# Kernel optimization log

Hardware: AMD Instinct MI355X
Metric: run time of the kernel (lower is better)

Reference implementation:

```python
import jax, jax.numpy as jnp
import numpy as np

TOP_K = 2


def setup_inputs() -> dict:
    key = jax.random.key(0)
    ks = jax.random.split(key, 4)
    T, E, D_IN, D_H, D_OUT = 8192, 8, 1024, 4096, 1024
    s_in = 1.0 / np.sqrt(D_IN)
    s_h = 1.0 / np.sqrt(D_H)
    return {
        "x": jax.random.normal(ks[0], (T, D_IN), dtype=jnp.float32),
        "Wg": jax.random.normal(ks[1], (D_IN, E), dtype=jnp.float32) * s_in,
        "bg": jnp.zeros((E,), dtype=jnp.float32),
        "W1": jax.random.normal(ks[2], (E, D_IN, D_H), dtype=jnp.float32) * s_in,
        "b1": jnp.zeros((E, D_H), dtype=jnp.float32),
        "W2": jax.random.normal(ks[3], (E, D_H, D_OUT), dtype=jnp.float32) * s_h,
        "b2": jnp.zeros((E, D_OUT), dtype=jnp.float32),
    }


def moe_forward(x, Wg, bg, W1, b1, W2, b2):
    # Top-k gate: logits [T,E] -> top-k -> softmax over the k selected logits,
    # scattered back into a dense [T,E] weight matrix (zeros elsewhere).
    logits = x @ Wg + bg                              # [T, E]
    topv, topi = jax.lax.top_k(logits, TOP_K)         # [T, k]
    topw = jax.nn.softmax(topv, axis=-1)              # [T, k]
    T, E = logits.shape
    weights = jnp.zeros((T, E), dtype=logits.dtype)
    rows = jnp.arange(T)[:, None]
    weights = weights.at[rows, topi].set(topw)        # dense gate weights [T, E]

    # Dense all-expert MLP (faithful to the naive torch module):
    h = jax.nn.relu(jnp.einsum("ti,eih->teh", x, W1) + b1[None])   # [T, E, H]
    expert_out = jnp.einsum("teh,eho->teo", h, W2) + b2[None]      # [T, E, O]

    # Top-k weighted sum over experts.
    return jnp.einsum("te,teo->to", weights, expert_out)           # [T, O]


def reference(x, Wg, bg, W1, b1, W2, b2):
    return moe_forward(x, Wg, bg, W1, b1, W2, b2)
```

## Files before the change

### kernel.cpp

```cpp
#include <hip/hip_runtime.h>
#include <hip/hip_bf16.h>
#include <stdint.h>

#define NTOK 8192
#define NE 8
#define DIN 1024
#define DH 4096
#define DOUT 1024
#define MAXMB 135

typedef __bf16 bf16;
typedef __bf16 bf16_8 __attribute__((ext_vector_type(8)));
typedef __bf16 bf16_4 __attribute__((ext_vector_type(4)));
typedef float f32_4 __attribute__((ext_vector_type(4)));

__device__ __forceinline__ void gl_lds16(const void* g, void* l) {
  __builtin_amdgcn_global_load_lds(
      (const __attribute__((address_space(1))) unsigned int*)g,
      (__attribute__((address_space(3))) unsigned int*)l, 16, 0, 0);
}

__global__ void gate_kernel(const float* __restrict__ x, const float* __restrict__ Wg,
                            const float* __restrict__ bg,
                            int* __restrict__ topi, float* __restrict__ topw) {
  int t = blockIdx.x * 4 + (threadIdx.x >> 6);
  int lane = threadIdx.x & 63;
  float acc[NE];
#pragma unroll
  for (int e = 0; e < NE; e++) acc[e] = 0.f;
  const float* xr = x + (size_t)t * DIN;
#pragma unroll
  for (int i = 0; i < DIN / 64; i++) {
    float xv = xr[lane + 64 * i];
    const float4* wr = (const float4*)(Wg + (size_t)(lane + 64 * i) * NE);
    float4 w0 = wr[0], w1 = wr[1];
    acc[0] += xv * w0.x; acc[1] += xv * w0.y; acc[2] += xv * w0.z; acc[3] += xv * w0.w;
    acc[4] += xv * w1.x; acc[5] += xv * w1.y; acc[6] += xv * w1.z; acc[7] += xv * w1.w;
  }
#pragma unroll
  for (int off = 32; off > 0; off >>= 1)
#pragma unroll
    for (int e = 0; e < NE; e++) acc[e] += __shfl_xor(acc[e], off, 64);
  if (lane == 0) {
    float lg[NE];
#pragma unroll
    for (int e = 0; e < NE; e++) lg[e] = acc[e] + bg[e];
    int i0 = 0; float v0 = lg[0];
#pragma unroll
    for (int e = 1; e < NE; e++) if (lg[e] > v0) { v0 = lg[e]; i0 = e; }
    int i1 = -1; float v1 = -3.0e38f;
#pragma unroll
    for (int e = 0; e < NE; e++) if (e != i0 && lg[e] > v1) { v1 = lg[e]; i1 = e; }
    float ex = expf(v1 - v0);
    float w0 = 1.f / (1.f + ex);
    float w1 = ex / (1.f + ex);
    topi[2 * t] = i0; topi[2 * t + 1] = i1;
    topw[2 * t] = w0; topw[2 * t + 1] = w1;
  }
}

__global__ void hist_kernel(const int* __restrict__ topi, int* __restrict__ counts,
                            int* __restrict__ pos) {
  __shared__ int bins[NE];
  __shared__ int base[NE];
  int tid = threadIdx.x;
  if (tid < NE) bins[tid] = 0;
  __syncthreads();
  int i = blockIdx.x * 256 + tid;
  int e = topi[i];
  int local = atomicAdd(&bins[e], 1);
  __syncthreads();
  if (tid < NE) base[tid] = atomicAdd(&counts[tid], bins[tid]);
  __syncthreads();
  pos[i] = base[e] + local;
}

__global__ void scan_kernel(const int* counts, int* offsets, int* mblk_off) {
  if (threadIdx.x == 0) {
    int s = 0, b = 0;
    for (int e = 0; e < NE; e++) {
      offsets[e] = s; mblk_off[e] = b;
      s += counts[e]; b += (counts[e] + 127) >> 7;
    }
    mblk_off[NE] = b;
  }
}

__global__ void pack_kernel(const int* __restrict__ topi, const float* __restrict__ topw,
                            const int* __restrict__ pos, const int* __restrict__ offsets,
                            int* __restrict__ tok_list, float* __restrict__ w_list) {
  int i = blockIdx.x * 256 + threadIdx.x;
  int e = topi[i];
  int slot = offsets[e] + pos[i];
  tok_list[slot] = i >> 1;
  w_list[slot] = topw[i];
}

__global__ void cvtx_kernel(const float* __restrict__ x, bf16* __restrict__ xb) {
  size_t i = ((size_t)blockIdx.x * 256 + threadIdx.x) * 8;
  float4 a = *(const float4*)(x + i);
  float4 b = *(const float4*)(x + i + 4);
  bf16_8 o;
  o[0] = (bf16)a.x; o[1] = (bf16)a.y; o[2] = (bf16)a.z; o[3] = (bf16)a.w;
  o[4] = (bf16)b.x; o[5] = (bf16)b.y; o[6] = (bf16)b.z; o[7] = (bf16)b.w;
  *(bf16_8*)(xb + i) = o;
}

__global__ void init_out_kernel(const int* __restrict__ topi, const float* __restrict__ topw,
                                const float* __restrict__ b2, float* __restrict__ out) {
  int t = blockIdx.x;
  int c = threadIdx.x * 4;
  int e0 = topi[2 * t], e1 = topi[2 * t + 1];
  float w0 = topw[2 * t], w1 = topw[2 * t + 1];
  float4 v0 = *(const float4*)(b2 + (size_t)e0 * DOUT + c);
  float4 v1 = *(const float4*)(b2 + (size_t)e1 * DOUT + c);
  float4 o;
  o.x = w0 * v0.x + w1 * v1.x;
  o.y = w0 * v0.y + w1 * v1.y;
  o.z = w0 * v0.z + w1 * v1.z;
  o.w = w0 * v0.w + w1 * v1.w;
  *(float4*)(out + (size_t)t * DOUT + c) = o;
}

__global__ void tcvt_kernel(const float* __restrict__ src, bf16* __restrict__ dst,
                            int src_ld, long long src_es, int dst_ld, long long dst_es) {
  __shared__ bf16 tile[32][33];
  const float* s = src + blockIdx.z * src_es + (size_t)(blockIdx.x * 32) * src_ld + blockIdx.y * 32;
  bf16* d = dst + blockIdx.z * dst_es + (size_t)(blockIdx.y * 32) * dst_ld + blockIdx.x * 32;
  int tid = threadIdx.x;
  int r = tid >> 3, c4 = (tid & 7) * 4;
  float4 v = *(const float4*)(s + (size_t)r * src_ld + c4);
  tile[r][c4] = (bf16)v.x; tile[r][c4 + 1] = (bf16)v.y;
  tile[r][c4 + 2] = (bf16)v.z; tile[r][c4 + 3] = (bf16)v.w;
  __syncthreads();
  int n = tid >> 3, k4 = (tid & 7) * 4;
  bf16_4 o;
  o[0] = tile[k4][n]; o[1] = tile[k4 + 1][n]; o[2] = tile[k4 + 2][n]; o[3] = tile[k4 + 3][n];
  *(bf16_4*)(d + (size_t)n * dst_ld + k4) = o;
}


__global__ __launch_bounds__(256) void gemm1_kernel(
    const bf16* __restrict__ xb, const bf16* __restrict__ W1t,
    const float* __restrict__ b1, const int* __restrict__ counts,
    const int* __restrict__ offsets, const int* __restrict__ mblk_off,
    const int* __restrict__ tok_list,
    bf16* __restrict__ h, int hchunk, int hc0) {
  int mb = blockIdx.y;
  if (mb >= mblk_off[NE]) return;
  int e = 0;
  while (mb >= mblk_off[e + 1]) e++;
  int ne = counts[e];
  int m0 = (mb - mblk_off[e]) * 128;
  int off = offsets[e];
  int n0 = blockIdx.x * 128;

  __shared__ bf16 ldsA[128 * 32];
  __shared__ bf16 ldsB[128 * 32];

  int tid = threadIdx.x;
  int w = tid >> 6, lane = tid & 63;
  int scol = (((lane & 3) ^ (lane >> 3)) & 3) * 8;

  const bf16* gA[2]; const bf16* gB[2];
  bf16* lA[2]; bf16* lB[2];
#pragma unroll
  for (int j = 0; j < 2; j++) {
    int seg = w * 2 + j;
    int row = seg * 16 + (lane >> 2);
    int slot = off + m0 + row;
    int smax = off + ne - 1;
    if (slot > smax) slot = smax;
    int tok = tok_list[slot];
    gA[j] = xb + (size_t)tok * DIN + scol;
    lA[j] = ldsA + seg * 512;
    gB[j] = W1t + ((size_t)e * hchunk + n0 + row) * DIN + scol;
    lB[j] = ldsB + seg * 512;
  }

  f32_4 acc[4][4];
#pragma unroll
  for (int i = 0; i < 4; i++)
#pragma unroll
    for (int j = 0; j < 4; j++) acc[i][j] = (f32_4){0.f, 0.f, 0.f, 0.f};

  int wm = w & 1, wn = w >> 1;
  int lr = lane & 15, quad = lane >> 4;
  int rcol = ((quad ^ (lr >> 1)) & 3) * 8;

  for (int kt = 0; kt < DIN / 32; kt++) {
#pragma unroll
    for (int j = 0; j < 2; j++) {
      gl_lds16(gA[j], lA[j]);
      gl_lds16(gB[j], lB[j]);
    }
    gA[0] += 32; gA[1] += 32; gB[0] += 32; gB[1] += 32;
    __syncthreads();
    bf16_8 af[4], bfr[4];
#pragma unroll
    for (int mt = 0; mt < 4; mt++)
      af[mt] = *(const bf16_8*)(ldsA + (wm * 64 + mt * 16 + lr) * 32 + rcol);
#pragma unroll
    for (int nt = 0; nt < 4; nt++)
      bfr[nt] = *(const bf16_8*)(ldsB + (wn * 64 + nt * 16 + lr) * 32 + rcol);
#pragma unroll
    for (int mt = 0; mt < 4; mt++)
#pragma unroll
      for (int nt = 0; nt < 4; nt++)
        acc[mt][nt] = __builtin_amdgcn_mfma_f32_16x16x32_bf16(af[mt], bfr[nt], acc[mt][nt], 0, 0, 0);
    __syncthreads();
  }

#pragma unroll
  for (int nt = 0; nt < 4; nt++) {
    int cloc = wn * 64 + nt * 16 + lr;
    int c = n0 + cloc;
    float bias = b1[(size_t)e * DH + hc0 + c];
#pragma unroll
    for (int mt = 0; mt < 4; mt++) {
#pragma unroll
      for (int r2 = 0; r2 < 4; r2++) {
        int row = wm * 64 + mt * 16 + quad * 4 + r2;
        if (m0 + row < ne) {
          float v = acc[mt][nt][r2] + bias;
          v = v > 0.f ? v : 0.f;
          h[(size_t)(off + m0 + row) * hchunk + c] = (bf16)v;
        }
      }
    }
  }
}

__global__ __launch_bounds__(256) void gemm2_kernel(
    const bf16* __restrict__ h, const bf16* __restrict__ W2t,
    const int* __restrict__ counts, const int* __restrict__ offsets,
    const int* __restrict__ mblk_off, const int* __restrict__ tok_list,
    const float* __restrict__ w_list,
    float* __restrict__ out, int hchunk) {
  int mb = blockIdx.y;
  if (mb >= mblk_off[NE]) return;
  int e = 0;
  while (mb >= mblk_off[e + 1]) e++;
  int ne = counts[e];
  int m0 = (mb - mblk_off[e]) * 128;
  int off = offsets[e];
  int n0 = blockIdx.x * 128;

  __shared__ bf16 ldsA[128 * 32];
  __shared__ bf16 ldsB[128 * 32];

  int tid = threadIdx.x;
  int w = tid >> 6, lane = tid & 63;
  int scol = (((lane & 3) ^ (lane >> 3)) & 3) * 8;

  const bf16* gA[2]; const bf16* gB[2];
  bf16* lA[2]; bf16* lB[2];
#pragma unroll
  for (int j = 0; j < 2; j++) {
    int seg = w * 2 + j;
    int row = seg * 16 + (lane >> 2);
    gA[j] = h + (size_t)(off + m0 + row) * hchunk + scol;
    lA[j] = ldsA + seg * 512;
    gB[j] = W2t + ((size_t)e * DOUT + n0 + row) * hchunk + scol;
    lB[j] = ldsB + seg * 512;
  }

  f32_4 acc[4][4];
#pragma unroll
  for (int i = 0; i < 4; i++)
#pragma unroll
    for (int j = 0; j < 4; j++) acc[i][j] = (f32_4){0.f, 0.f, 0.f, 0.f};

  int wm = w & 1, wn = w >> 1;
  int lr = lane & 15, quad = lane >> 4;
  int rcol = ((quad ^ (lr >> 1)) & 3) * 8;

  for (int kt = 0; kt < hchunk / 32; kt++) {
#pragma unroll
    for (int j = 0; j < 2; j++) {
      gl_lds16(gA[j], lA[j]);
      gl_lds16(gB[j], lB[j]);
    }
    gA[0] += 32; gA[1] += 32; gB[0] += 32; gB[1] += 32;
    __syncthreads();
    bf16_8 af[4], bfr[4];
#pragma unroll
    for (int mt = 0; mt < 4; mt++)
      af[mt] = *(const bf16_8*)(ldsA + (wm * 64 + mt * 16 + lr) * 32 + rcol);
#pragma unroll
    for (int nt = 0; nt < 4; nt++)
      bfr[nt] = *(const bf16_8*)(ldsB + (wn * 64 + nt * 16 + lr) * 32 + rcol);
#pragma unroll
    for (int mt = 0; mt < 4; mt++)
#pragma unroll
      for (int nt = 0; nt < 4; nt++)
        acc[mt][nt] = __builtin_amdgcn_mfma_f32_16x16x32_bf16(af[mt], bfr[nt], acc[mt][nt], 0, 0, 0);
    __syncthreads();
  }

#pragma unroll
  for (int mt = 0; mt < 4; mt++) {
#pragma unroll
    for (int r2 = 0; r2 < 4; r2++) {
      int row = wm * 64 + mt * 16 + quad * 4 + r2;
      if (m0 + row < ne) {
        int slot = off + m0 + row;
        int t = tok_list[slot];
        float wgt = w_list[slot];
        float* orow = out + (size_t)t * DOUT;
#pragma unroll
        for (int nt = 0; nt < 4; nt++) {
          int c = n0 + wn * 64 + nt * 16 + lr;
          atomicAdd(orow + c, wgt * acc[mt][nt][r2]);
        }
      }
    }
  }
}

extern "C" void kernel_launch(void* const* d_in, const int* in_sizes, int n_in,
                              void* d_out, int out_size, void* d_ws, size_t ws_size,
                              hipStream_t stream) {
  const float* x  = (const float*)d_in[0];
  const float* Wg = (const float*)d_in[1];
  const float* bg = (const float*)d_in[2];
  const float* W1 = (const float*)d_in[3];
  const float* b1 = (const float*)d_in[4];
  const float* W2 = (const float*)d_in[5];
  const float* b2 = (const float*)d_in[6];
  float* out = (float*)d_out;

  char* p = (char*)d_ws;
  int*   counts   = (int*)p;   p += 256;
  int*   offsets  = (int*)p;   p += 256;
  int*   mblk_off = (int*)p;   p += 256;
  int*   topi     = (int*)p;   p += 16384 * 4;
  float* topw     = (float*)p; p += 16384 * 4;
  int*   pos      = (int*)p;   p += 16384 * 4;
  int*   tok_list = (int*)p;   p += 16384 * 4;
  float* w_list   = (float*)p; p += 16384 * 4;
  bf16*  xb       = (bf16*)p;  p += (size_t)NTOK * DIN * 2;

  size_t fixedBytes = (size_t)(p - (char*)d_ws);
  int hchunk = 2048;
  while (hchunk > 128 && fixedBytes + (size_t)hchunk * 65792 > ws_size) hchunk >>= 1;

  bf16* W1t  = (bf16*)p; p += (size_t)NE * hchunk * DIN * 2;
  bf16* W2t  = (bf16*)p; p += (size_t)NE * DOUT * hchunk * 2;
  bf16* hbuf = (bf16*)p; p += (size_t)(16384 + 128) * hchunk * 2;

  hipMemsetAsync(counts, 0, 32, stream);
  gate_kernel<<<NTOK / 4, 256, 0, stream>>>(x, Wg, bg, topi, topw);
  cvtx_kernel<<<(NTOK * DIN) / (8 * 256), 256, 0, stream>>>(x, xb);
  hist_kernel<<<64, 256, 0, stream>>>(topi, counts, pos);
  scan_kernel<<<1, 64, 0, stream>>>(counts, offsets, mblk_off);
  pack_kernel<<<64, 256, 0, stream>>>(topi, topw, pos, offsets, tok_list, w_list);
  init_out_kernel<<<NTOK, 256, 0, stream>>>(topi, topw, b2, out);

  int nchunks = DH / hchunk;
  for (int c = 0; c < nchunks; c++) {
    int hc0 = c * hchunk;
    tcvt_kernel<<<dim3(DIN / 32, hchunk / 32, NE), 256, 0, stream>>>(
        W1 + hc0, W1t, DH, (long long)DIN * DH, DIN, (long long)hchunk * DIN);
    tcvt_kernel<<<dim3(hchunk / 32, DOUT / 32, NE), 256, 0, stream>>>(
        W2 + (size_t)hc0 * DOUT, W2t, DOUT, (long long)DH * DOUT, hchunk, (long long)DOUT * hchunk);
    gemm1_kernel<<<dim3(hchunk / 128, MAXMB), 256, 0, stream>>>(
        xb, W1t, b1, counts, offsets, mblk_off, tok_list, hbuf, hchunk, hc0);
    gemm2_kernel<<<dim3(DOUT / 128, MAXMB), 256, 0, stream>>>(
        hbuf, W2t, counts, offsets, mblk_off, tok_list, w_list, out, hchunk);
  }
}
```

Before: 900.7 us.

## Replace atomic scatter in gemm2 with slot-ordered buffer and combine kernel

gemm2 now writes plain stores into a per-slot fp32 buffer laid out in expert-sorted order, instead of weighted atomicAdds into token rows of the output. A new combine kernel gathers each token's two expert rows, adds the biases, applies the gate weights and writes the output, replacing init_out. The default hidden chunk is raised to 4096 so that, if the workspace is large enough, a single pass avoids read-modify-write accumulation. This costs an extra 64MB intermediate buffer plus a gather pass, and needs more workspace.

```diff
diff --git a/kernel.cpp b/kernel.cpp
--- a/kernel.cpp
+++ b/kernel.cpp
@@ -86,14 +86,14 @@
   }
 }
 
-__global__ void pack_kernel(const int* __restrict__ topi, const float* __restrict__ topw,
+__global__ void pack_kernel(const int* __restrict__ topi,
                             const int* __restrict__ pos, const int* __restrict__ offsets,
-                            int* __restrict__ tok_list, float* __restrict__ w_list) {
+                            int* __restrict__ tok_list, int* __restrict__ slot_of) {
   int i = blockIdx.x * 256 + threadIdx.x;
   int e = topi[i];
   int slot = offsets[e] + pos[i];
   tok_list[slot] = i >> 1;
-  w_list[slot] = topw[i];
+  slot_of[i] = slot;
 }
 
 __global__ void cvtx_kernel(const float* __restrict__ x, bf16* __restrict__ xb) {
@@ -104,22 +104,6 @@
   o[0] = (bf16)a.x; o[1] = (bf16)a.y; o[2] = (bf16)a.z; o[3] = (bf16)a.w;
   o[4] = (bf16)b.x; o[5] = (bf16)b.y; o[6] = (bf16)b.z; o[7] = (bf16)b.w;
   *(bf16_8*)(xb + i) = o;
-}
-
-__global__ void init_out_kernel(const int* __restrict__ topi, const float* __restrict__ topw,
-                                const float* __restrict__ b2, float* __restrict__ out) {
-  int t = blockIdx.x;
-  int c = threadIdx.x * 4;
-  int e0 = topi[2 * t], e1 = topi[2 * t + 1];
-  float w0 = topw[2 * t], w1 = topw[2 * t + 1];
-  float4 v0 = *(const float4*)(b2 + (size_t)e0 * DOUT + c);
-  float4 v1 = *(const float4*)(b2 + (size_t)e1 * DOUT + c);
-  float4 o;
-  o.x = w0 * v0.x + w1 * v1.x;
-  o.y = w0 * v0.y + w1 * v1.y;
-  o.z = w0 * v0.z + w1 * v1.z;
-  o.w = w0 * v0.w + w1 * v1.w;
-  *(float4*)(out + (size_t)t * DOUT + c) = o;
 }
 
 __global__ void tcvt_kernel(const float* __restrict__ src, bf16* __restrict__ dst,
@@ -234,9 +218,8 @@
 __global__ __launch_bounds__(256) void gemm2_kernel(
     const bf16* __restrict__ h, const bf16* __restrict__ W2t,
     const int* __restrict__ counts, const int* __restrict__ offsets,
-    const int* __restrict__ mblk_off, const int* __restrict__ tok_list,
-    const float* __restrict__ w_list,
-    float* __restrict__ out, int hchunk) {
+    const int* __restrict__ mblk_off,
+    float* __restrict__ y, int hchunk, int accum) {
   int mb = blockIdx.y;
   if (mb >= mblk_off[NE]) return;
   int e = 0;
@@ -304,18 +287,37 @@
     for (int r2 = 0; r2 < 4; r2++) {
       int row = wm * 64 + mt * 16 + quad * 4 + r2;
       if (m0 + row < ne) {
-        int slot = off + m0 + row;
-        int t = tok_list[slot];
-        float wgt = w_list[slot];
-        float* orow = out + (size_t)t * DOUT;
+        float* yrow = y + (size_t)(off + m0 + row) * DOUT + n0;
 #pragma unroll
         for (int nt = 0; nt < 4; nt++) {
-          int c = n0 + wn * 64 + nt * 16 + lr;
-          atomicAdd(orow + c, wgt * acc[mt][nt][r2]);
+          int c = wn * 64 + nt * 16 + lr;
+          float v = acc[mt][nt][r2];
+          if (accum) v += yrow[c];
+          yrow[c] = v;
         }
       }
     }
   }
+}
+
+__global__ void combine_kernel(const int* __restrict__ topi, const float* __restrict__ topw,
+                               const int* __restrict__ slot_of, const float* __restrict__ y,
+                               const float* __restrict__ b2, float* __restrict__ out) {
+  int t = blockIdx.x;
+  int c = threadIdx.x * 4;
+  int e0 = topi[2 * t], e1 = topi[2 * t + 1];
+  float w0 = topw[2 * t], w1 = topw[2 * t + 1];
+  int s0 = slot_of[2 * t], s1 = slot_of[2 * t + 1];
+  float4 a = *(const float4*)(y + (size_t)s0 * DOUT + c);
+  float4 b = *(const float4*)(y + (size_t)s1 * DOUT + c);
+  float4 p = *(const float4*)(b2 + (size_t)e0 * DOUT + c);
+  float4 q = *(const float4*)(b2 + (size_t)e1 * DOUT + c);
+  float4 o;
+  o.x = w0 * (a.x + p.x) + w1 * (b.x + q.x);
+  o.y = w0 * (a.y + p.y) + w1 * (b.y + q.y);
+  o.z = w0 * (a.z + p.z) + w1 * (b.z + q.z);
+  o.w = w0 * (a.w + p.w) + w1 * (b.w + q.w);
+  *(float4*)(out + (size_t)t * DOUT + c) = o;
 }
 
 extern "C" void kernel_launch(void* const* d_in, const int* in_sizes, int n_in,
@@ -338,11 +340,12 @@
   float* topw     = (float*)p; p += 16384 * 4;
   int*   pos      = (int*)p;   p += 16384 * 4;
   int*   tok_list = (int*)p;   p += 16384 * 4;
-  float* w_list   = (float*)p; p += 16384 * 4;
+  int*   slot_of  = (int*)p;   p += 16384 * 4;
   bf16*  xb       = (bf16*)p;  p += (size_t)NTOK * DIN * 2;
+  float* y        = (float*)p; p += (size_t)16384 * DOUT * 4;
 
   size_t fixedBytes = (size_t)(p - (char*)d_ws);
-  int hchunk = 2048;
+  int hchunk = 4096;
   while (hchunk > 128 && fixedBytes + (size_t)hchunk * 65792 > ws_size) hchunk >>= 1;
 
   bf16* W1t  = (bf16*)p; p += (size_t)NE * hchunk * DIN * 2;
@@ -354,8 +357,7 @@
   cvtx_kernel<<<(NTOK * DIN) / (8 * 256), 256, 0, stream>>>(x, xb);
   hist_kernel<<<64, 256, 0, stream>>>(topi, counts, pos);
   scan_kernel<<<1, 64, 0, stream>>>(counts, offsets, mblk_off);
-  pack_kernel<<<64, 256, 0, stream>>>(topi, topw, pos, offsets, tok_list, w_list);
-  init_out_kernel<<<NTOK, 256, 0, stream>>>(topi, topw, b2, out);
+  pack_kernel<<<64, 256, 0, stream>>>(topi, pos, offsets, tok_list, slot_of);
 
   int nchunks = DH / hchunk;
   for (int c = 0; c < nchunks; c++) {
@@ -367,6 +369,7 @@
     gemm1_kernel<<<dim3(hchunk / 128, MAXMB), 256, 0, stream>>>(
         xb, W1t, b1, counts, offsets, mblk_off, tok_list, hbuf, hchunk, hc0);
     gemm2_kernel<<<dim3(DOUT / 128, MAXMB), 256, 0, stream>>>(
-        hbuf, W2t, counts, offsets, mblk_off, tok_list, w_list, out, hchunk);
-  }
-}
+        hbuf, W2t, counts, offsets, mblk_off, y, hchunk, c > 0 ? 1 : 0);
+  }
+  combine_kernel<<<NTOK, 256, 0, stream>>>(topi, topw, slot_of, y, b2, out);
+}
```

Result: no change. 889.9 us (-1.2%).
